# Performance work log

Hardware: AMD Instinct MI355X
Metric: run time of the kernel (lower is better)

The kernel has to match this reference:

```python
import jax, jax.numpy as jnp
import numpy as np

B = 32        # graphs per batch
MAXN = 2048   # max nodes per graph (dense batch length)
HEADS = 8
DH = 64       # head dim (512/8)
M = 256       # FAVOR+ random features
D = 512
EPS = 1e-5    # batchnorm eps
KEPS = 1e-6   # performer stabilizer


def _batchnorm(x, g, b):
    # torch BatchNorm1d training-mode: biased batch statistics over node dim
    mu = jnp.mean(x, axis=0)
    var = jnp.mean((x - mu) ** 2, axis=0)
    return (x - mu) * jax.lax.rsqrt(var + EPS) * g + b


def setup_inputs() -> dict:
    key = jax.random.key(0)
    ks = jax.random.split(key, 10)
    sizes = 1024 + (np.arange(B) * 131) % 1025   # ragged graph sizes in [1024, 2048]
    N = int(sizes.sum())                          # 48544
    E = N * 8
    batch = jnp.asarray(np.repeat(np.arange(B), sizes), dtype=jnp.int32)
    edge_index = jax.random.randint(ks[0], (2, E), 0, N, dtype=jnp.int32)
    s = 1.0 / np.sqrt(D)
    return {
        'x': jax.random.normal(ks[1], (N, D), jnp.float32),
        'batch': batch,
        'edge_index': edge_index,
        'norm1_g': jnp.ones((D,), jnp.float32),
        'norm1_b': jnp.zeros((D,), jnp.float32),
        'norm2_g': jnp.ones((D,), jnp.float32),
        'norm2_b': jnp.zeros((D,), jnp.float32),
        'W_conv': jax.random.normal(ks[2], (D, D), jnp.float32) * s,
        'b_conv': jnp.zeros((D,), jnp.float32),
        'Wq': jax.random.normal(ks[3], (D, D), jnp.float32) * s,
        'Wk': jax.random.normal(ks[4], (D, D), jnp.float32) * s,
        'Wv': jax.random.normal(ks[5], (D, D), jnp.float32) * s,
        'Wo': jax.random.normal(ks[6], (D, D), jnp.float32) * s,
        'proj': jax.random.normal(ks[7], (M, DH), jnp.float32),
    }


def _forward(x, batch, edge_index, norm1_g, norm1_b, norm2_g, norm2_b,
             W_conv, b_conv, Wq, Wk, Wv, Wo, proj):
    N = x.shape[0]
    E = edge_index.shape[1]
    h = x

    # norm1 (+ dropout p=0 -> identity) then local GNN conv (mean-agg GCN + linear + relu)
    xn = _batchnorm(x, norm1_g, norm1_b)
    msg = xn[edge_index[0]]                                        # [E, D] gather
    agg = jax.ops.segment_sum(msg, edge_index[1], num_segments=N)  # [N, D] scatter-add
    deg = jax.ops.segment_sum(jnp.ones((E,), x.dtype), edge_index[1], num_segments=N)
    agg = agg / jnp.maximum(deg, 1.0)[:, None]
    conv_out = jax.nn.relu(agg @ W_conv + b_conv)

    # to_dense_batch(h, batch) -> h_dense [B, MAXN, D], mask [B, MAXN]
    counts = jax.ops.segment_sum(jnp.ones((N,), jnp.int32), batch, num_segments=B)
    offsets = jnp.concatenate([jnp.zeros((1,), jnp.int32), jnp.cumsum(counts)[:-1]])
    pos = jnp.arange(N, dtype=jnp.int32) - offsets[batch]
    h_dense = jnp.zeros((B, MAXN, D), x.dtype).at[batch, pos].set(h)
    mask = jnp.zeros((B, MAXN), bool).at[batch, pos].set(True)

    # Performer FAVOR+ non-causal self-attention
    def heads(t, W):
        return (t @ W).reshape(B, MAXN, HEADS, DH).transpose(0, 2, 1, 3)  # [B,H,MAXN,DH]
    q, k, v = heads(h_dense, Wq), heads(h_dense, Wk), heads(h_dense, Wv)

    scale = DH ** -0.25  # data normalizer applied to q and k each

    def phi(t, is_query):
        t = t * scale
        u = jnp.einsum('bhnd,md->bhnm', t, proj)           # [B,H,MAXN,M]
        diag = 0.5 * jnp.sum(t * t, axis=-1, keepdims=True)
        if is_query:
            m_ = jnp.max(u, axis=-1, keepdims=True)
        else:
            m_ = jnp.max(u, axis=(-2, -1), keepdims=True)
        return jnp.exp(u - diag - jax.lax.stop_gradient(m_)) / np.sqrt(M) + KEPS

    qf = phi(q, True)
    kf = phi(k, False) * mask[:, None, :, None]   # zero padded keys
    vm = v * mask[:, None, :, None]

    kv = jnp.einsum('bhnm,bhnd->bhmd', kf, vm)                    # [B,H,M,DH]
    z = 1.0 / (jnp.einsum('bhnm,bhm->bhn', qf, kf.sum(axis=2)) + KEPS)
    attn = jnp.einsum('bhnm,bhmd->bhnd', qf, kv) * z[..., None]   # [B,H,MAXN,DH]
    attn = attn.transpose(0, 2, 1, 3).reshape(B, MAXN, D) @ Wo

    h_attn = attn[batch, pos]                                      # gather back: [mask]

    return _batchnorm(conv_out + h_attn + h, norm2_g, norm2_b)


def reference(x, batch, edge_index, norm1_g, norm1_b, norm2_g, norm2_b,
              W_conv, b_conv, Wq, Wk, Wv, Wo, proj):
    return _forward(x, batch, edge_index, norm1_g, norm1_b, norm2_g, norm2_b,
                    W_conv, b_conv, Wq, Wk, Wv, Wo, proj)
```

## Files before the change

### kernel.cpp

```cpp
#include <hip/hip_runtime.h>
#include <stdint.h>

#define CDIV(a,b) (((a)+(b)-1)/(b))

typedef __attribute__((ext_vector_type(4))) float f32x4;
typedef __attribute__((ext_vector_type(8))) short s16x8;
typedef __attribute__((ext_vector_type(8))) unsigned short u16x8;
typedef __attribute__((ext_vector_type(4))) unsigned short u16x4;

__device__ __forceinline__ float bf2f(unsigned short u) {
  union { unsigned int i; float f; } c; c.i = ((unsigned int)u) << 16; return c.f;
}
__device__ __forceinline__ unsigned short f2bf(float f) {
  union { float f; unsigned int i; } c; c.f = f;
  unsigned int u = c.i;
  u += 0x7fffu + ((u >> 16) & 1u);
  return (unsigned short)(u >> 16);
}

#define KVROWS 80

template<int BM, int BN, int WM, int WN, int EPI, int GSWAP>
__global__ __launch_bounds__(256) void gemm_bt(
    const unsigned short* __restrict__ A, const unsigned short* __restrict__ B,
    void* __restrict__ Cout, const float* __restrict__ aux,
    int K, int lda, int ldb, int ldc, long zsC, int Mstore)
{
  constexpr int MT = BM / (WM * 16);
  constexpr int NT = BN / (WN * 16);
  constexpr int LDT = 40;
  __shared__ unsigned short As[BM * LDT];
  __shared__ unsigned short Bs[BN * LDT];
  const int tid = threadIdx.x, wid = tid >> 6, lane = tid & 63;
  const int l15 = lane & 15, hi = lane >> 4;
  const int wr = wid / WN, wc = wid % WN;
  const int bx = GSWAP ? blockIdx.y : blockIdx.x;
  const int by = GSWAP ? blockIdx.x : blockIdx.y;
  long m0 = (long)by * BM;
  const int n0 = bx * BN;
  f32x4 acc[MT][NT] = {};
  for (int k0 = 0; k0 < K; k0 += 32) {
    #pragma unroll
    for (int c = tid; c < BM * 4; c += 256) {
      int row = c >> 2, c8 = (c & 3) * 8;
      *(u16x8*)(&As[row * LDT + c8]) = *(const u16x8*)(A + (m0 + row) * lda + k0 + c8);
    }
    #pragma unroll
    for (int c = tid; c < BN * 4; c += 256) {
      int row = c >> 2, c8 = (c & 3) * 8;
      *(u16x8*)(&Bs[row * LDT + c8]) = *(const u16x8*)(B + (long)(n0 + row) * ldb + k0 + c8);
    }
    __syncthreads();
    s16x8 af[MT], bfv[NT];
    #pragma unroll
    for (int mt = 0; mt < MT; mt++)
      af[mt] = *(const s16x8*)(&As[(wr * MT * 16 + mt * 16 + l15) * LDT + hi * 8]);
    #pragma unroll
    for (int nt = 0; nt < NT; nt++)
      bfv[nt] = *(const s16x8*)(&Bs[(wc * NT * 16 + nt * 16 + l15) * LDT + hi * 8]);
    #pragma unroll
    for (int mt = 0; mt < MT; mt++)
      #pragma unroll
      for (int nt = 0; nt < NT; nt++)
        acc[mt][nt] = __builtin_amdgcn_mfma_f32_16x16x32_bf16(bfv[nt], af[mt], acc[mt][nt], 0, 0, 0);
    __syncthreads();
  }
  #pragma unroll
  for (int mt = 0; mt < MT; mt++) {
    long r = m0 + wr * (MT * 16) + mt * 16 + l15;
    if (r < Mstore) {
      #pragma unroll
      for (int nt = 0; nt < NT; nt++) {
        const int col0 = n0 + wc * (NT * 16) + nt * 16 + hi * 4;
        f32x4 v = acc[mt][nt];
        if constexpr (EPI == 5) {
          float* cp = (float*)Cout + r * ldc + col0;
          f32x4 cur = *(f32x4*)cp;
          #pragma unroll
          for (int i = 0; i < 4; i++) {
            float o = v[i] + aux[col0 + i];
            cur[i] += o > 0.f ? o : 0.f;
          }
          *(f32x4*)cp = cur;
        } else if constexpr (EPI == 7) {
          u16x4 o;
          #pragma unroll
          for (int i = 0; i < 4; i++) o[i] = f2bf(v[i]);
          *(u16x4*)((unsigned short*)Cout + (long)(col0 >> 6) * zsC + r * 64 + (col0 & 63)) = o;
        } else if constexpr (EPI == 8) {
          const f32x4 ax = *(const f32x4*)(aux + r * ldc + col0);
          f32x4 o;
          #pragma unroll
          for (int i = 0; i < 4; i++) o[i] = v[i] + ax[i];
          *(f32x4*)((float*)Cout + r * ldc + col0) = o;
        }
      }
    }
  }
}

__global__ __launch_bounds__(256) void k_kmax(
    const unsigned short* __restrict__ kvqh, const unsigned short* __restrict__ projb,
    const unsigned int* __restrict__ offs, unsigned int* __restrict__ kmax, long Npad) {
  __shared__ float wmax[4];
  const int tid = threadIdx.x, wid = tid >> 6, lane = tid & 63;
  const int bh = blockIdx.x & 255, xb = blockIdx.x >> 8;
  const int b = bh >> 3, h = bh & 7;
  const unsigned int off = offs[b];
  const int nb = (int)(offs[b + 1] - off);
  const int m0 = xb * 64;
  if (m0 >= nb) return;
  const unsigned short* A = kvqh + ((long)(8 + h) * Npad + off + m0) * 64;
  f32x4 acc[4][4] = {};
  #pragma unroll
  for (int k0 = 0; k0 < 64; k0 += 32) {
    s16x8 af[4], bfv[4];
    #pragma unroll
    for (int mt = 0; mt < 4; mt++)
      af[mt] = *(const s16x8*)(A + (long)(mt * 16 + (lane & 15)) * 64 + k0 + ((lane >> 4) * 8));
    #pragma unroll
    for (int nt = 0; nt < 4; nt++)
      bfv[nt] = *(const s16x8*)(projb + (long)(wid * 64 + nt * 16 + (lane & 15)) * 64 + k0 + ((lane >> 4) * 8));
    #pragma unroll
    for (int mt = 0; mt < 4; mt++)
      #pragma unroll
      for (int nt = 0; nt < 4; nt++)
        acc[mt][nt] = __builtin_amdgcn_mfma_f32_16x16x32_bf16(af[mt], bfv[nt], acc[mt][nt], 0, 0, 0);
  }
  float bm = -3.0e38f;
  #pragma unroll
  for (int mt = 0; mt < 4; mt++)
    #pragma unroll
    for (int i = 0; i < 4; i++) {
      int row = mt * 16 + ((lane >> 4) << 2) + i;
      if (m0 + row < nb) {
        #pragma unroll
        for (int nt = 0; nt < 4; nt++) bm = fmaxf(bm, acc[mt][nt][i]);
      }
    }
  #pragma unroll
  for (int s = 1; s < 64; s <<= 1) bm = fmaxf(bm, __shfl_xor(bm, s));
  if (lane == 0) wmax[wid] = bm;
  __syncthreads();
  if (tid == 0) {
    float m = fmaxf(fmaxf(wmax[0], wmax[1]), fmaxf(wmax[2], wmax[3]));
    atomicMax(&kmax[b * 8 + h], __float_as_uint(fmaxf(m, 0.f)));
  }
}

__global__ __launch_bounds__(256) void k_kvm(
    const unsigned short* __restrict__ kvqh, const unsigned short* __restrict__ projb,
    const unsigned int* __restrict__ offs, const unsigned int* __restrict__ kmax,
    unsigned short* __restrict__ kvTb, long Npad) {
  constexpr int TLD = 72;
  __shared__ unsigned short vsT[2][64 * TLD];
  __shared__ unsigned short kfsT[64 * TLD];
  const int tid = threadIdx.x, wid = tid >> 6, lane = tid & 63;
  const int bh = blockIdx.x & 255, mblk = blockIdx.x >> 8;
  const int b = bh >> 3, h = bh & 7;
  const unsigned int off = offs[b];
  const int nb = (int)(offs[b + 1] - off);
  const float km = __uint_as_float(kmax[b * 8 + h]);
  const unsigned short* Kp = kvqh + ((long)(8 + h) * Npad + off) * 64;
  const unsigned short* Vp = kvqh + ((long)(16 + h) * Npad + off) * 64;
  const unsigned short* Pp = projb + (long)(mblk * 64 + wid * 16) * 64;
  const int l15 = lane & 15, hi = lane >> 4;
  const int mloc = wid * 16 + l15;

  #pragma unroll
  for (int c = tid; c < 512; c += 256) {
    int row = c >> 3, c8 = (c & 7) * 8;
    int rot = (c & 7) * 8;
    u16x8 v = *(const u16x8*)(Vp + (long)row * 64 + c8);
    #pragma unroll
    for (int j = 0; j < 8; j++) vsT[0][(c8 + j) * TLD + ((row + rot) & 63)] = v[j];
  }
  __syncthreads();

  f32x4 akv[4] = {};
  float ksum = 0.f;
  int buf = 0;
  for (int n0 = 0; n0 < nb; n0 += 64) {
    f32x4 acc[4] = {};
    float dsum[4] = {0.f, 0.f, 0.f, 0.f};
    #pragma unroll
    for (int k0 = 0; k0 < 64; k0 += 32) {
      s16x8 af[4];
      #pragma unroll
      for (int mt = 0; mt < 4; mt++)
        af[mt] = *(const s16x8*)(Kp + ((long)n0 + mt * 16 + l15) * 64 + k0 + hi * 8);
      s16x8 bfv = *(const s16x8*)(Pp + (long)l15 * 64 + k0 + hi * 8);
      #pragma unroll
      for (int mt = 0; mt < 4; mt++) {
        #pragma unroll
        for (int j = 0; j < 8; j++) {
          float a = bf2f((unsigned short)af[mt][j]);
          dsum[mt] += a * a;
        }
        acc[mt] = __builtin_amdgcn_mfma_f32_16x16x32_bf16(af[mt], bfv, acc[mt], 0, 0, 0);
      }
    }
    float rs[4];
    #pragma unroll
    for (int mt = 0; mt < 4; mt++) {
      float s = dsum[mt];
      s += __shfl_xor(s, 16); s += __shfl_xor(s, 32);
      rs[mt] = 0.0625f * s;
    }
    #pragma unroll
    for (int mt = 0; mt < 4; mt++) {
      int r0 = mt * 16 + hi * 4;
      float e[4];
      #pragma unroll
      for (int i = 0; i < 4; i++) {
        float dg = __shfl(rs[mt], hi * 4 + i);
        e[i] = (n0 + r0 + i < nb) ? (__expf(acc[mt][i] - dg - km) * 0.0625f + 1e-6f) : 0.f;
      }
      ksum += e[0] + e[1] + e[2] + e[3];
      unsigned int p0 = (unsigned int)f2bf(e[0]) | ((unsigned int)f2bf(e[1]) << 16);
      unsigned int p1 = (unsigned int)f2bf(e[2]) | ((unsigned int)f2bf(e[3]) << 16);
      *(unsigned int*)(&kfsT[mloc * TLD + r0]) = p0;
      *(unsigned int*)(&kfsT[mloc * TLD + r0 + 2]) = p1;
    }
    if (n0 + 64 < nb) {
      #pragma unroll
      for (int c = tid; c < 512; c += 256) {
        int row = c >> 3, c8 = (c & 7) * 8;
        int rot = (c & 7) * 8;
        u16x8 v = *(const u16x8*)(Vp + ((long)n0 + 64 + row) * 64 + c8);
        #pragma unroll
        for (int j = 0; j < 8; j++) vsT[buf ^ 1][(c8 + j) * TLD + ((row + rot) & 63)] = v[j];
      }
    }
    #pragma unroll
    for (int ks = 0; ks < 2; ks++) {
      s16x8 bB = *(const s16x8*)(&kfsT[mloc * TLD + ks * 32 + hi * 8]);
      #pragma unroll
      for (int mt2 = 0; mt2 < 4; mt2++) {
        int d = mt2 * 16 + l15;
        int rrot = ((ks * 32 + hi * 8) + ((d >> 3) & 7) * 8) & 63;
        s16x8 aA = *(const s16x8*)(&vsT[buf][d * TLD + rrot]);
        akv[mt2] = __builtin_amdgcn_mfma_f32_16x16x32_bf16(aA, bB, akv[mt2], 0, 0, 0);
      }
    }
    __syncthreads();
    buf ^= 1;
  }
  long base = ((long)b * 8 + h) * (KVROWS * 256);
  const int m = mblk * 64 + mloc;
  #pragma unroll
  for (int mt2 = 0; mt2 < 4; mt2++)
    #pragma unroll
    for (int i = 0; i < 4; i++) {
      int d = mt2 * 16 + hi * 4 + i;
      kvTb[base + (long)d * 256 + m] = f2bf(akv[mt2][i]);
    }
  ksum += __shfl_xor(ksum, 16); ksum += __shfl_xor(ksum, 32);
  if (hi == 0) kvTb[base + 64 * 256 + m] = f2bf(ksum);
}

__global__ __launch_bounds__(256) void k_qflash(
    const unsigned short* __restrict__ qh_all, const unsigned short* __restrict__ projb,
    const unsigned short* __restrict__ kvTb, const unsigned int* __restrict__ offs,
    unsigned short* __restrict__ attn, long Npad) {
  constexpr int QLDT = 264;
  __shared__ unsigned short qfs[64 * QLDT];
  __shared__ float sdiag[64];
  __shared__ float smax[4][64];
  const int tid = threadIdx.x, wid = tid >> 6, lane = tid & 63;
  const int l15 = lane & 15, hi = lane >> 4;
  const int bh = blockIdx.x & 255, xb = blockIdx.x >> 8;
  const int b = bh >> 3, h = bh & 7;
  const unsigned int off = offs[b];
  const int nb = (int)(offs[b + 1] - off);
  const int m0 = xb * 64;
  if (m0 >= nb) return;
  const unsigned short* A = qh_all + ((long)h * Npad + off + m0) * 64;
  f32x4 acc[4][4] = {};
  float dsum[4] = {0.f, 0.f, 0.f, 0.f};
  #pragma unroll
  for (int k0 = 0; k0 < 64; k0 += 32) {
    s16x8 af[4], bfv[4];
    #pragma unroll
    for (int mt = 0; mt < 4; mt++)
      af[mt] = *(const s16x8*)(A + (long)(mt * 16 + l15) * 64 + k0 + hi * 8);
    #pragma unroll
    for (int nt = 0; nt < 4; nt++)
      bfv[nt] = *(const s16x8*)(projb + (long)(wid * 64 + nt * 16 + l15) * 64 + k0 + hi * 8);
    if (wid == 0) {
      #pragma unroll
      for (int mt = 0; mt < 4; mt++)
        #pragma unroll
        for (int j = 0; j < 8; j++) {
          float a = bf2f((unsigned short)af[mt][j]);
          dsum[mt] += a * a;
        }
    }
    #pragma unroll
    for (int mt = 0; mt < 4; mt++)
      #pragma unroll
      for (int nt = 0; nt < 4; nt++)
        acc[mt][nt] = __builtin_amdgcn_mfma_f32_16x16x32_bf16(af[mt], bfv[nt], acc[mt][nt], 0, 0, 0);
  }
  if (wid == 0) {
    #pragma unroll
    for (int mt = 0; mt < 4; mt++) {
      float s = dsum[mt];
      s += __shfl_xor(s, 16); s += __shfl_xor(s, 32);
      if (lane < 16) sdiag[mt * 16 + lane] = 0.0625f * s;
    }
  }
  #pragma unroll
  for (int mt = 0; mt < 4; mt++)
    #pragma unroll
    for (int i = 0; i < 4; i++) {
      float rm = fmaxf(fmaxf(acc[mt][0][i], acc[mt][1][i]), fmaxf(acc[mt][2][i], acc[mt][3][i]));
      rm = fmaxf(rm, __shfl_xor(rm, 1)); rm = fmaxf(rm, __shfl_xor(rm, 2));
      rm = fmaxf(rm, __shfl_xor(rm, 4)); rm = fmaxf(rm, __shfl_xor(rm, 8));
      if (l15 == 0) smax[wid][mt * 16 + hi * 4 + i] = rm;
    }
  __syncthreads();
  #pragma unroll
  for (int mt = 0; mt < 4; mt++)
    #pragma unroll
    for (int i = 0; i < 4; i++) {
      int row = mt * 16 + hi * 4 + i;
      float rm = fmaxf(fmaxf(smax[0][row], smax[1][row]), fmaxf(smax[2][row], smax[3][row]));
      float sub = sdiag[row] + rm;
      #pragma unroll
      for (int nt = 0; nt < 4; nt++) {
        int col = wid * 64 + nt * 16 + l15;
        qfs[row * QLDT + col] = f2bf(__expf(acc[mt][nt][i] - sub) * 0.0625f + 1e-6f);
      }
    }
  __syncthreads();
  const unsigned short* kvb = kvTb + ((long)b * 8 + h) * (KVROWS * 256);
  f32x4 acc2[4] = {};
  f32x4 acc3 = {};
  #pragma unroll
  for (int ks = 0; ks < 8; ks++) {
    s16x8 aq = *(const s16x8*)(&qfs[(wid * 16 + l15) * QLDT + ks * 32 + hi * 8]);
    #pragma unroll
    for (int t = 0; t < 4; t++) {
      s16x8 bk = *(const s16x8*)(kvb + (long)(t * 16 + l15) * 256 + ks * 32 + hi * 8);
      acc2[t] = __builtin_amdgcn_mfma_f32_16x16x32_bf16(aq, bk, acc2[t], 0, 0, 0);
    }
    s16x8 bz = *(const s16x8*)(kvb + (long)(64 + l15) * 256 + ks * 32 + hi * 8);
    acc3 = __builtin_amdgcn_mfma_f32_16x16x32_bf16(aq, bz, acc3, 0, 0, 0);
  }
  float zr[4];
  #pragma unroll
  for (int i = 0; i < 4; i++) {
    float zden = __shfl(acc3[i], hi * 16);
    zr[i] = 1.f / (zden + 1e-6f);
  }
  #pragma unroll
  for (int t = 0; t < 4; t++)
    #pragma unroll
    for (int i = 0; i < 4; i++) {
      int row = wid * 16 + hi * 4 + i;
      if (m0 + row < nb)
        attn[(long)(off + m0 + row) * 512 + h * 64 + t * 16 + l15] = f2bf(acc2[t][i] * zr[i]);
    }
}


__global__ void k_fill(float* __restrict__ out, long n, float v) {
  long i = (long)blockIdx.x * 256 + threadIdx.x;
  if (i < n) out[i] = v;
}

__global__ void k_convx_stats(const float* __restrict__ x, unsigned short* __restrict__ xb,
                              float* __restrict__ s1, float* __restrict__ s2, int N, int rpb) {
  int t = threadIdx.x;
  int r0 = blockIdx.x * rpb;
  int r1 = min(N, r0 + rpb);
  float a1 = 0, a2 = 0, b1 = 0, b2 = 0;
  for (int r = r0; r < r1; r++) {
    const float* xr = x + (long)r * 512 + 2 * t;
    float va = xr[0], vb = xr[1];
    a1 += va; a2 += va * va; b1 += vb; b2 += vb * vb;
    *(unsigned int*)(xb + (long)r * 512 + 2 * t) =
        (unsigned int)f2bf(va) | ((unsigned int)f2bf(vb) << 16);
  }
  atomicAdd(&s1[2 * t], a1); atomicAdd(&s2[2 * t], a2);
  atomicAdd(&s1[2 * t + 1], b1); atomicAdd(&s2[2 * t + 1], b2);
}

__global__ void k_transall(const float* __restrict__ w0, const float* __restrict__ w1,
                           const float* __restrict__ w2, const float* __restrict__ w3,
                           const float* __restrict__ w4, unsigned short* __restrict__ out) {
  long idx = (long)blockIdx.x * 256 + threadIdx.x;
  if (idx >= (5L << 18)) return;
  int which = (int)(idx >> 18);
  int r = (int)(idx & 262143);
  int n = r >> 9, k = r & 511;
  const float* w = which == 0 ? w0 : which == 1 ? w1 : which == 2 ? w2 : which == 3 ? w3 : w4;
  out[idx] = f2bf(w[k * 512 + n]);
}

__global__ void k_scale_copy_bf(const float* __restrict__ in, unsigned short* __restrict__ out,
                                int n, float scl) {
  int i = blockIdx.x * 256 + threadIdx.x;
  if (i < n) out[i] = f2bf(in[i] * scl);
}

__global__ void k_bn_final(const float* __restrict__ s1, const float* __restrict__ s2,
                           const float* __restrict__ g, const float* __restrict__ b,
                           float* __restrict__ a, float* __restrict__ c, float invN) {
  int t = threadIdx.x;
  float mu = s1[t] * invN;
  float var = s2[t] * invN - mu * mu;
  float inv = rsqrtf(var + 1e-5f);
  float av = g[t] * inv;
  a[t] = av;
  c[t] = b[t] - mu * av;
}

__global__ void k_deg(const int* __restrict__ ed, unsigned int* __restrict__ deg, long E) {
  long i = (long)blockIdx.x * 256 + threadIdx.x;
  if (i < E) atomicAdd(&deg[ed[i]], 1u);
}

__global__ void k_offs(const int* __restrict__ batch, unsigned int* __restrict__ offs, int N) {
  int i = blockIdx.x * 256 + threadIdx.x;
  if (i >= N) return;
  int b = batch[i];
  if (i == 0) { for (int bb = 0; bb <= b; bb++) offs[bb] = 0; }
  else {
    int pb = batch[i - 1];
    if (pb != b) for (int bb = pb + 1; bb <= b; bb++) offs[bb] = i;
  }
  if (i == N - 1) { for (int bb = b + 1; bb <= 32; bb++) offs[bb] = N; }
}

__global__ __launch_bounds__(1024) void k_scan_nodes(const unsigned int* __restrict__ deg,
                                                     unsigned int* __restrict__ rowstart, int N) {
  __shared__ unsigned int wsum[16];
  __shared__ unsigned int carry_s;
  int t = threadIdx.x, lane = t & 63, wid = t >> 6;
  if (t == 0) carry_s = 0;
  __syncthreads();
  for (int base = 0; base < N; base += 1024) {
    int i = base + t;
    unsigned int v = (i < N) ? deg[i] : 0;
    unsigned int sc = v;
    #pragma unroll
    for (int s = 1; s < 64; s <<= 1) {
      unsigned int u = __shfl_up(sc, s);
      if (lane >= s) sc += u;
    }
    if (lane == 63) wsum[wid] = sc;
    __syncthreads();
    unsigned int woff = 0, tot = 0;
    #pragma unroll
    for (int w = 0; w < 16; w++) { unsigned int s = wsum[w]; if (w < wid) woff += s; tot += s; }
    unsigned int carry = carry_s;
    if (i < N) rowstart[i] = carry + woff + sc - v;
    __syncthreads();
    if (t == 0) carry_s = carry + tot;
    __syncthreads();
  }
  if (threadIdx.x == 0) rowstart[N] = carry_s;
}

__global__ void k_csr_fill(const int* __restrict__ es, const int* __restrict__ ed,
                           const unsigned int* __restrict__ rowstart,
                           unsigned int* __restrict__ cursor, int* __restrict__ csr, long E) {
  long e = (long)blockIdx.x * 256 + threadIdx.x;
  if (e >= E) return;
  int d = ed[e];
  unsigned int slot = atomicAdd(&cursor[d], 1u);
  csr[rowstart[d] + slot] = es[e];
}

__global__ __launch_bounds__(128) void k_gather(const int* __restrict__ csr,
                                                const unsigned int* __restrict__ rowstart,
                                                const float* __restrict__ x,
                                                const float* __restrict__ a1, const float* __restrict__ c1,
                                                unsigned short* __restrict__ conv_in, int N) {
  long n = blockIdx.x;
  int c = threadIdx.x * 4;
  u16x4 o; o[0] = 0; o[1] = 0; o[2] = 0; o[3] = 0;
  if (n < N) {
    unsigned int r0 = rowstart[n], r1 = rowstart[n + 1];
    if (r1 > r0) {
      f32x4 acc0 = {}, acc1 = {};
      unsigned int j = r0;
      for (; j + 2 <= r1; j += 2) {
        int s0 = csr[j], s1 = csr[j + 1];
        acc0 += *(const f32x4*)(x + (long)s0 * 512 + c);
        acc1 += *(const f32x4*)(x + (long)s1 * 512 + c);
      }
      if (j < r1) { int s0 = csr[j]; acc0 += *(const f32x4*)(x + (long)s0 * 512 + c); }
      f32x4 acc = acc0 + acc1;
      float inv = 1.f / (float)(r1 - r0);
      o[0] = f2bf(acc[0] * inv * a1[c + 0] + c1[c + 0]);
      o[1] = f2bf(acc[1] * inv * a1[c + 1] + c1[c + 1]);
      o[2] = f2bf(acc[2] * inv * a1[c + 2] + c1[c + 2]);
      o[3] = f2bf(acc[3] * inv * a1[c + 3] + c1[c + 3]);
    }
  }
  *(u16x4*)(conv_in + n * 512 + c) = o;
}

__global__ void k_stats(const float* __restrict__ y, float* __restrict__ s1,
                        float* __restrict__ s2, int N, int rpb) {
  int t = threadIdx.x;
  int r0 = blockIdx.x * rpb;
  int r1 = min(N, r0 + rpb);
  float a1 = 0, a2 = 0, b1 = 0, b2 = 0;
  for (int r = r0; r < r1; r++) {
    float va = y[(long)r * 512 + t];
    float vb = y[(long)r * 512 + t + 256];
    a1 += va; a2 += va * va; b1 += vb; b2 += vb * vb;
  }
  atomicAdd(&s1[t], a1); atomicAdd(&s2[t], a2);
  atomicAdd(&s1[t + 256], b1); atomicAdd(&s2[t + 256], b2);
}

__global__ void k_bn_apply(float* __restrict__ y, const float* __restrict__ a,
                           const float* __restrict__ c, long total) {
  long i4 = ((long)blockIdx.x * 256 + threadIdx.x) * 4;
  if (i4 >= total) return;
  int col = (int)(i4 & 511);
  f32x4 v = *(const f32x4*)(y + i4);
  #pragma unroll
  for (int j = 0; j < 4; j++) v[j] = v[j] * a[col + j] + c[col + j];
  *(f32x4*)(y + i4) = v;
}


extern "C" void kernel_launch(void* const* d_in, const int* in_sizes, int n_in,
                              void* d_out, int out_size, void* d_ws, size_t ws_size,
                              hipStream_t stream) {
  (void)n_in; (void)out_size;
  const float* x = (const float*)d_in[0];
  const int* batch = (const int*)d_in[1];
  const int* eidx = (const int*)d_in[2];
  const float* n1g = (const float*)d_in[3];
  const float* n1b = (const float*)d_in[4];
  const float* n2g = (const float*)d_in[5];
  const float* n2b = (const float*)d_in[6];
  const float* wconv = (const float*)d_in[7];
  const float* bconv = (const float*)d_in[8];
  const float* wq = (const float*)d_in[9];
  const float* wk = (const float*)d_in[10];
  const float* wv = (const float*)d_in[11];
  const float* wo = (const float*)d_in[12];
  const float* proj = (const float*)d_in[13];

  const int N = in_sizes[1];
  const long E = in_sizes[2] / 2;
  const long Npad = CDIV(N, 128) * 128 + 256;
  const int Mb = (int)((CDIV(N, 128) * 128 + 128) / 128);
  const int* es = eidx;
  const int* ed = eidx + E;
  float* out = (float*)d_out;

  char* p = (char*)d_ws;
  auto alloc = [&](size_t bytes) -> char* {
    char* r = p;
    p += (bytes + 255) & ~(size_t)255;
    return r;
  };
  unsigned short* kvqh = (unsigned short*)alloc((size_t)24 * Npad * 64 * 2);
  unsigned short* xbf  = (unsigned short*)alloc((size_t)Npad * 512 * 2);
  unsigned short* kvT_b = (unsigned short*)alloc((size_t)32 * 8 * KVROWS * 256 * 2);
  unsigned short* wts   = (unsigned short*)alloc((size_t)5 * 512 * 512 * 2);
  unsigned short* proj_s = (unsigned short*)alloc((size_t)256 * 64 * 2);
  float* bn1_acc = (float*)alloc(1024 * 4);
  float* bn1_ac  = (float*)alloc(1024 * 4);
  float* bn2_acc = (float*)alloc(1024 * 4);
  float* bn2_ac  = (float*)alloc(1024 * 4);
  unsigned int* deg      = (unsigned int*)alloc((size_t)N * 4);
  unsigned int* offs     = (unsigned int*)alloc(33 * 4);
  unsigned int* kmax     = (unsigned int*)alloc(32 * 8 * 4);
  unsigned int* rowstart = (unsigned int*)alloc((size_t)(N + 1) * 4);
  unsigned int* cursor   = (unsigned int*)alloc((size_t)N * 4);
  int* csr               = (int*)alloc((size_t)E * 4);
  size_t required = (size_t)(p - (char*)d_ws);
  if (required > ws_size) {
    k_fill<<<(int)CDIV((long)N * 512, 256), 256, 0, stream>>>(
        out, (long)N * 512, 1.0e6f + (float)(ws_size >> 20));
    return;
  }
  unsigned short* wqkv_t  = wts;
  unsigned short* wconv_t = wts + 3 * 512 * 512;
  unsigned short* wo_t    = wts + 4 * 512 * 512;
  unsigned short* attn_all = xbf;
  unsigned short* conv_in  = xbf;

  hipMemsetAsync(deg, 0, (size_t)N * 4, stream);
  hipMemsetAsync(cursor, 0, (size_t)N * 4, stream);
  hipMemsetAsync(kmax, 0, 32 * 8 * 4, stream);
  hipMemsetAsync(bn1_acc, 0, 1024 * 4, stream);
  hipMemsetAsync(bn2_acc, 0, 1024 * 4, stream);
  hipMemsetAsync(kvT_b, 0, (size_t)32 * 8 * KVROWS * 256 * 2, stream);
  hipMemsetAsync(xbf + (size_t)N * 512, 0, (size_t)(Npad - N) * 512 * 2, stream);

  int rpb = CDIV(N, 1024);
  k_convx_stats<<<1024, 256, 0, stream>>>(x, xbf, bn1_acc, bn1_acc + 512, N, rpb);
  k_transall<<<(int)CDIV(5L << 18, 256), 256, 0, stream>>>(wq, wk, wv, wconv, wo, wts);
  k_scale_copy_bf<<<CDIV(256 * 64, 256), 256, 0, stream>>>(proj, proj_s, 256 * 64, 0.35355339059327373f);
  k_bn_final<<<1, 512, 0, stream>>>(bn1_acc, bn1_acc + 512, n1g, n1b, bn1_ac, bn1_ac + 512, 1.f / N);
  k_deg<<<(int)CDIV(E, 256), 256, 0, stream>>>(ed, deg, E);
  k_offs<<<CDIV(N, 256), 256, 0, stream>>>(batch, offs, N);
  k_scan_nodes<<<1, 1024, 0, stream>>>(deg, rowstart, N);
  k_csr_fill<<<(int)CDIV(E, 256), 256, 0, stream>>>(es, ed, rowstart, cursor, csr, E);

  gemm_bt<128, 128, 2, 2, 7, 1><<<dim3(Mb, 12), 256, 0, stream>>>(
      xbf, wqkv_t, kvqh, nullptr, 512, 512, 512, 0, (long)Npad * 64, (int)Npad);

  k_kmax<<<32 * 256, 256, 0, stream>>>(kvqh, proj_s, offs, kmax, Npad);
  k_kvm<<<4 * 256, 256, 0, stream>>>(kvqh, proj_s, offs, kmax, kvT_b, Npad);

  k_qflash<<<32 * 256, 256, 0, stream>>>(
      kvqh, proj_s, kvT_b, offs, attn_all, Npad);

  gemm_bt<128, 128, 2, 2, 8, 0><<<dim3(4, Mb), 256, 0, stream>>>(
      attn_all, wo_t, out, x, 512, 512, 512, 512, 0, N);

  k_gather<<<(int)(CDIV(N, 128) * 128), 128, 0, stream>>>(csr, rowstart, x, bn1_ac, bn1_ac + 512, conv_in, N);
  gemm_bt<128, 128, 2, 2, 5, 0><<<dim3(4, Mb), 256, 0, stream>>>(
      conv_in, wconv_t, out, bconv, 512, 512, 512, 512, 0, N);

  k_stats<<<1024, 256, 0, stream>>>(out, bn2_acc, bn2_acc + 512, N, rpb);
  k_bn_final<<<1, 512, 0, stream>>>(bn2_acc, bn2_acc + 512, n2g, n2b, bn2_ac, bn2_ac + 512, 1.f / N);
  k_bn_apply<<<(int)CDIV((long)N * 512 / 4, 256), 256, 0, stream>>>(out, bn2_ac, bn2_ac + 512, (long)N * 512);
}
```

Baseline: 1.144 ms.

## Fuse output and conv GEMMs with residual and batchnorm statistics

Replaces the separate Wo GEMM, conv GEMM and stats pass with one kernel. It computes both products per output tile, applies bias, ReLU and the residual, writes the output once and accumulates the batchnorm sums through shuffles and atomics. Attention output now lives in a separate buffer so the gather can run before qflash, and the kvT memset is dropped. Occupancy hints are added to kmax and qflash. The fused kernel doubles shared memory and accumulator registers, which may reduce occupancy.

```diff
diff --git a/kernel.cpp b/kernel.cpp
--- a/kernel.cpp
+++ b/kernel.cpp
@@ -73,33 +73,115 @@
       for (int nt = 0; nt < NT; nt++) {
         const int col0 = n0 + wc * (NT * 16) + nt * 16 + hi * 4;
         f32x4 v = acc[mt][nt];
-        if constexpr (EPI == 5) {
-          float* cp = (float*)Cout + r * ldc + col0;
-          f32x4 cur = *(f32x4*)cp;
-          #pragma unroll
-          for (int i = 0; i < 4; i++) {
-            float o = v[i] + aux[col0 + i];
-            cur[i] += o > 0.f ? o : 0.f;
-          }
-          *(f32x4*)cp = cur;
-        } else if constexpr (EPI == 7) {
+        if constexpr (EPI == 7) {
           u16x4 o;
           #pragma unroll
           for (int i = 0; i < 4; i++) o[i] = f2bf(v[i]);
           *(u16x4*)((unsigned short*)Cout + (long)(col0 >> 6) * zsC + r * 64 + (col0 & 63)) = o;
-        } else if constexpr (EPI == 8) {
-          const f32x4 ax = *(const f32x4*)(aux + r * ldc + col0);
-          f32x4 o;
-          #pragma unroll
-          for (int i = 0; i < 4; i++) o[i] = v[i] + ax[i];
-          *(f32x4*)((float*)Cout + r * ldc + col0) = o;
         }
       }
     }
   }
 }
 
-__global__ __launch_bounds__(256) void k_kmax(
+__global__ __launch_bounds__(256) void gemm_out_fused(
+    const unsigned short* __restrict__ A1, const unsigned short* __restrict__ B1,
+    const unsigned short* __restrict__ A2, const unsigned short* __restrict__ B2,
+    float* __restrict__ out, const float* __restrict__ x, const float* __restrict__ bias,
+    float* __restrict__ s1, float* __restrict__ s2, int Mstore)
+{
+  constexpr int LDT = 40;
+  __shared__ unsigned short As1[128 * LDT];
+  __shared__ unsigned short Bs1[128 * LDT];
+  __shared__ unsigned short As2[128 * LDT];
+  __shared__ unsigned short Bs2[128 * LDT];
+  const int tid = threadIdx.x, wid = tid >> 6, lane = tid & 63;
+  const int l15 = lane & 15, hi = lane >> 4;
+  const int wr = wid >> 1, wc = wid & 1;
+  long m0 = (long)blockIdx.x * 128;
+  const int n0 = blockIdx.y * 128;
+  f32x4 acc1[4][4] = {};
+  f32x4 acc2[4][4] = {};
+  for (int k0 = 0; k0 < 512; k0 += 32) {
+    #pragma unroll
+    for (int c = tid; c < 512; c += 256) {
+      int row = c >> 2, c8 = (c & 3) * 8;
+      *(u16x8*)(&As1[row * LDT + c8]) = *(const u16x8*)(A1 + (m0 + row) * 512 + k0 + c8);
+      *(u16x8*)(&Bs1[row * LDT + c8]) = *(const u16x8*)(B1 + (long)(n0 + row) * 512 + k0 + c8);
+      *(u16x8*)(&As2[row * LDT + c8]) = *(const u16x8*)(A2 + (m0 + row) * 512 + k0 + c8);
+      *(u16x8*)(&Bs2[row * LDT + c8]) = *(const u16x8*)(B2 + (long)(n0 + row) * 512 + k0 + c8);
+    }
+    __syncthreads();
+    {
+      s16x8 af[4], bfv[4];
+      #pragma unroll
+      for (int mt = 0; mt < 4; mt++)
+        af[mt] = *(const s16x8*)(&As1[(wr * 64 + mt * 16 + l15) * LDT + hi * 8]);
+      #pragma unroll
+      for (int nt = 0; nt < 4; nt++)
+        bfv[nt] = *(const s16x8*)(&Bs1[(wc * 64 + nt * 16 + l15) * LDT + hi * 8]);
+      #pragma unroll
+      for (int mt = 0; mt < 4; mt++)
+        #pragma unroll
+        for (int nt = 0; nt < 4; nt++)
+          acc1[mt][nt] = __builtin_amdgcn_mfma_f32_16x16x32_bf16(bfv[nt], af[mt], acc1[mt][nt], 0, 0, 0);
+    }
+    {
+      s16x8 af[4], bfv[4];
+      #pragma unroll
+      for (int mt = 0; mt < 4; mt++)
+        af[mt] = *(const s16x8*)(&As2[(wr * 64 + mt * 16 + l15) * LDT + hi * 8]);
+      #pragma unroll
+      for (int nt = 0; nt < 4; nt++)
+        bfv[nt] = *(const s16x8*)(&Bs2[(wc * 64 + nt * 16 + l15) * LDT + hi * 8]);
+      #pragma unroll
+      for (int mt = 0; mt < 4; mt++)
+        #pragma unroll
+        for (int nt = 0; nt < 4; nt++)
+          acc2[mt][nt] = __builtin_amdgcn_mfma_f32_16x16x32_bf16(bfv[nt], af[mt], acc2[mt][nt], 0, 0, 0);
+    }
+    __syncthreads();
+  }
+  float st[4][4] = {};
+  float sq[4][4] = {};
+  #pragma unroll
+  for (int mt = 0; mt < 4; mt++) {
+    long r = m0 + wr * 64 + mt * 16 + l15;
+    bool valid = r < Mstore;
+    #pragma unroll
+    for (int nt = 0; nt < 4; nt++) {
+      const int col0 = n0 + wc * 64 + nt * 16 + hi * 4;
+      f32x4 o = {0.f, 0.f, 0.f, 0.f};
+      if (valid) {
+        f32x4 xv = *(const f32x4*)(x + r * 512 + col0);
+        #pragma unroll
+        for (int i = 0; i < 4; i++) {
+          float cv = acc2[mt][nt][i] + bias[col0 + i];
+          cv = cv > 0.f ? cv : 0.f;
+          o[i] = acc1[mt][nt][i] + xv[i] + cv;
+        }
+        *(f32x4*)(out + r * 512 + col0) = o;
+      }
+      #pragma unroll
+      for (int i = 0; i < 4; i++) { st[nt][i] += o[i]; sq[nt][i] += o[i] * o[i]; }
+    }
+  }
+  #pragma unroll
+  for (int nt = 0; nt < 4; nt++)
+    #pragma unroll
+    for (int i = 0; i < 4; i++) {
+      float a = st[nt][i], b = sq[nt][i];
+      a += __shfl_xor(a, 1); a += __shfl_xor(a, 2); a += __shfl_xor(a, 4); a += __shfl_xor(a, 8);
+      b += __shfl_xor(b, 1); b += __shfl_xor(b, 2); b += __shfl_xor(b, 4); b += __shfl_xor(b, 8);
+      if (l15 == 0) {
+        const int col = n0 + wc * 64 + nt * 16 + hi * 4 + i;
+        atomicAdd(&s1[col], a);
+        atomicAdd(&s2[col], b);
+      }
+    }
+}
+
+__global__ __launch_bounds__(256, 4) void k_kmax(
     const unsigned short* __restrict__ kvqh, const unsigned short* __restrict__ projb,
     const unsigned int* __restrict__ offs, unsigned int* __restrict__ kmax, long Npad) {
   __shared__ float wmax[4];
@@ -259,7 +341,7 @@
   if (hi == 0) kvTb[base + 64 * 256 + m] = f2bf(ksum);
 }
 
-__global__ __launch_bounds__(256) void k_qflash(
+__global__ __launch_bounds__(256, 4) void k_qflash(
     const unsigned short* __restrict__ qh_all, const unsigned short* __restrict__ projb,
     const unsigned short* __restrict__ kvTb, const unsigned int* __restrict__ offs,
     unsigned short* __restrict__ attn, long Npad) {
@@ -504,21 +586,6 @@
   *(u16x4*)(conv_in + n * 512 + c) = o;
 }
 
-__global__ void k_stats(const float* __restrict__ y, float* __restrict__ s1,
-                        float* __restrict__ s2, int N, int rpb) {
-  int t = threadIdx.x;
-  int r0 = blockIdx.x * rpb;
-  int r1 = min(N, r0 + rpb);
-  float a1 = 0, a2 = 0, b1 = 0, b2 = 0;
-  for (int r = r0; r < r1; r++) {
-    float va = y[(long)r * 512 + t];
-    float vb = y[(long)r * 512 + t + 256];
-    a1 += va; a2 += va * va; b1 += vb; b2 += vb * vb;
-  }
-  atomicAdd(&s1[t], a1); atomicAdd(&s2[t], a2);
-  atomicAdd(&s1[t + 256], b1); atomicAdd(&s2[t + 256], b2);
-}
-
 __global__ void k_bn_apply(float* __restrict__ y, const float* __restrict__ a,
                            const float* __restrict__ c, long total) {
   long i4 = ((long)blockIdx.x * 256 + threadIdx.x) * 4;
@@ -554,6 +621,7 @@
   const long E = in_sizes[2] / 2;
   const long Npad = CDIV(N, 128) * 128 + 256;
   const int Mb = (int)((CDIV(N, 128) * 128 + 128) / 128);
+  const int MbO = CDIV(N, 128);
   const int* es = eidx;
   const int* ed = eidx + E;
   float* out = (float*)d_out;
@@ -588,15 +656,14 @@
   unsigned short* wqkv_t  = wts;
   unsigned short* wconv_t = wts + 3 * 512 * 512;
   unsigned short* wo_t    = wts + 4 * 512 * 512;
-  unsigned short* attn_all = xbf;
-  unsigned short* conv_in  = xbf;
+  unsigned short* attn2   = kvqh + (size_t)8 * Npad * 64;
+  unsigned short* conv_in = xbf;
 
   hipMemsetAsync(deg, 0, (size_t)N * 4, stream);
   hipMemsetAsync(cursor, 0, (size_t)N * 4, stream);
   hipMemsetAsync(kmax, 0, 32 * 8 * 4, stream);
   hipMemsetAsync(bn1_acc, 0, 1024 * 4, stream);
   hipMemsetAsync(bn2_acc, 0, 1024 * 4, stream);
-  hipMemsetAsync(kvT_b, 0, (size_t)32 * 8 * KVROWS * 256 * 2, stream);
   hipMemsetAsync(xbf + (size_t)N * 512, 0, (size_t)(Npad - N) * 512 * 2, stream);
 
   int rpb = CDIV(N, 1024);
@@ -615,17 +682,14 @@
   k_kmax<<<32 * 256, 256, 0, stream>>>(kvqh, proj_s, offs, kmax, Npad);
   k_kvm<<<4 * 256, 256, 0, stream>>>(kvqh, proj_s, offs, kmax, kvT_b, Npad);
 
+  k_gather<<<(int)(CDIV(N, 128) * 128), 128, 0, stream>>>(csr, rowstart, x, bn1_ac, bn1_ac + 512, conv_in, N);
+
   k_qflash<<<32 * 256, 256, 0, stream>>>(
-      kvqh, proj_s, kvT_b, offs, attn_all, Npad);
-
-  gemm_bt<128, 128, 2, 2, 8, 0><<<dim3(4, Mb), 256, 0, stream>>>(
-      attn_all, wo_t, out, x, 512, 512, 512, 512, 0, N);
-
-  k_gather<<<(int)(CDIV(N, 128) * 128), 128, 0, stream>>>(csr, rowstart, x, bn1_ac, bn1_ac + 512, conv_in, N);
-  gemm_bt<128, 128, 2, 2, 5, 0><<<dim3(4, Mb), 256, 0, stream>>>(
-      conv_in, wconv_t, out, bconv, 512, 512, 512, 512, 0, N);
-
-  k_stats<<<1024, 256, 0, stream>>>(out, bn2_acc, bn2_acc + 512, N, rpb);
+      kvqh, proj_s, kvT_b, offs, attn2, Npad);
+
+  gemm_out_fused<<<dim3(MbO, 4), 256, 0, stream>>>(
+      attn2, wo_t, conv_in, wconv_t, out, x, bconv, bn2_acc, bn2_acc + 512, N);
+
   k_bn_final<<<1, 512, 0, stream>>>(bn2_acc, bn2_acc + 512, n2g, n2b, bn2_ac, bn2_ac + 512, 1.f / N);
   k_bn_apply<<<(int)CDIV((long)N * 512 / 4, 256), 256, 0, stream>>>(out, bn2_ac, bn2_ac + 512, (long)N * 512);
 }
```

Measured after the change: 1.239 ms. 1.08x slower.
